# Optimization experiments

Measured on AMD Instinct MI355X. Metric: run time of the kernel, lower is better.

## Reference

```python
import jax, jax.numpy as jnp
import numpy as np

EPS = 1e-5
HEADS = 4


def _ln(x, s, b):
    m = jnp.mean(x, axis=-1, keepdims=True)
    v = jnp.mean(jnp.square(x - m), axis=-1, keepdims=True)
    return (x - m) * jax.lax.rsqrt(v + EPS) * s + b


def _gru(x, Wg, bg, Wcx, bcx, Wch, bch):
    # In this GRUCell the gates depend only on the inputs, so the gate and
    # candidate_x matmuls are precomputed over all timesteps; only the
    # (reset*h) @ Wch matmul is sequential.
    gx = jax.nn.sigmoid(x @ Wg + bg)   # [B,S,2H]
    cx = x @ Wcx + bcx                 # [B,S,H]
    H = Wch.shape[0]

    def step(h, gc):
        g, c = gc
        r, u = jnp.split(g, 2, axis=-1)
        cand = jnp.tanh(c + (r * h) @ Wch + bch)
        h_new = u * h + (1.0 - u) * cand
        return h_new, h_new

    h0 = jnp.zeros((x.shape[0], H), x.dtype)
    _, ys = jax.lax.scan(step, h0, (gx.transpose(1, 0, 2), cx.transpose(1, 0, 2)))
    return ys.transpose(1, 0, 2)


def _attn(x, s, b, Wq, bq, Wk, bk, Wv, bv, Wo, bo):
    skip = x
    xn = _ln(x, s, b)
    B, S, _ = xn.shape
    QKV = Wq.shape[1]
    hd = QKV // HEADS
    q = (xn @ Wq + bq).reshape(B, S, HEADS, hd)
    k = (xn @ Wk + bk).reshape(B, S, HEADS, hd)
    v = (xn @ Wv + bv).reshape(B, S, HEADS, hd)
    scores = jnp.einsum('bqhd,bkhd->bhqk', q, k) / jnp.sqrt(jnp.asarray(hd, x.dtype))
    probs = jax.nn.softmax(scores, axis=-1)
    o = jnp.einsum('bhqk,bkhd->bqhd', probs, v).reshape(B, S, QKV)
    return o @ Wo + bo + skip


def _forward(x_cgm, x_other, W_in, b_in, ln0_s, ln0_b,
             g0_Wg, g0_bg, g0_Wcx, g0_bcx, g0_Wch, g0_bch, ln1_s, ln1_b,
             g1_Wg, g1_bg, g1_Wcx, g1_bcx, g1_Wch, g1_bch, ln2_s, ln2_b,
             aln_s, aln_b, Wq, bq, Wk, bk, Wv, bv, Wo, bo,
             Wd1, bd1, lnd1_s, lnd1_b, Wd2, bd2, lnd2_s, lnd2_b, Wout, bout):
    # input projection + LN
    x = _ln(x_cgm @ W_in + b_in, ln0_s, ln0_b)
    # GRU block 0 (residual: dims match, 256==256)
    y = _gru(x, g0_Wg, g0_bg, g0_Wcx, g0_bcx, g0_Wch, g0_bch)
    x = _ln(y, ln1_s, ln1_b) + x
    # GRU block 1
    y = _gru(x, g1_Wg, g1_bg, g1_Wcx, g1_bcx, g1_Wch, g1_bch)
    x = _ln(y, ln2_s, ln2_b) + x
    # attention block after every 2nd GRU block
    x = _attn(x, aln_s, aln_b, Wq, bq, Wk, bk, Wv, bv, Wo, bo)
    # pool over time, concat static features, dense head (no residuals: dims differ)
    pooled = jnp.mean(x, axis=1)
    c = jnp.concatenate([pooled, x_other], axis=-1)
    c = _ln(jax.nn.relu(c @ Wd1 + bd1), lnd1_s, lnd1_b)
    c = _ln(jax.nn.relu(c @ Wd2 + bd2), lnd2_s, lnd2_b)
    return (c @ Wout + bout).squeeze(-1)


def setup_inputs() -> dict:
    key = jax.random.key(0)
    ks = iter(jax.random.split(key, 64))

    def nrm(shape, scale=1.0):
        return jax.random.normal(next(ks), shape, jnp.float32) * scale

    B, S, Fc, Fo, D, QKV = 64, 288, 16, 32, 256, 64
    inp = {
        'x_cgm': nrm((B, S, Fc)),
        'x_other': nrm((B, Fo)),
        'W_in': nrm((Fc, D), Fc ** -0.5), 'b_in': jnp.zeros((D,), jnp.float32),
        'ln0_s': jnp.ones((D,), jnp.float32), 'ln0_b': jnp.zeros((D,), jnp.float32),
    }
    for p in ('g0', 'g1'):
        inp[p + '_Wg'] = nrm((D, 2 * D), D ** -0.5)
        inp[p + '_bg'] = jnp.zeros((2 * D,), jnp.float32)
        inp[p + '_Wcx'] = nrm((D, D), D ** -0.5)
        inp[p + '_bcx'] = jnp.zeros((D,), jnp.float32)
        inp[p + '_Wch'] = nrm((D, D), D ** -0.5)
        inp[p + '_bch'] = jnp.zeros((D,), jnp.float32)
    for n in ('ln1', 'ln2', 'aln'):
        inp[n + '_s'] = jnp.ones((D,), jnp.float32)
        inp[n + '_b'] = jnp.zeros((D,), jnp.float32)
    for n in ('Wq', 'Wk', 'Wv'):
        inp[n] = nrm((D, QKV), D ** -0.5)
    for n in ('bq', 'bk', 'bv'):
        inp[n] = jnp.zeros((QKV,), jnp.float32)
    inp['Wo'] = nrm((QKV, D), QKV ** -0.5)
    inp['bo'] = jnp.zeros((D,), jnp.float32)
    inp['Wd1'] = nrm((D + Fo, 128), (D + Fo) ** -0.5)
    inp['bd1'] = jnp.zeros((128,), jnp.float32)
    inp['lnd1_s'] = jnp.ones((128,), jnp.float32)
    inp['lnd1_b'] = jnp.zeros((128,), jnp.float32)
    inp['Wd2'] = nrm((128, 64), 128 ** -0.5)
    inp['bd2'] = jnp.zeros((64,), jnp.float32)
    inp['lnd2_s'] = jnp.ones((64,), jnp.float32)
    inp['lnd2_b'] = jnp.zeros((64,), jnp.float32)
    inp['Wout'] = nrm((64, 1), 64 ** -0.5)
    inp['bout'] = jnp.zeros((1,), jnp.float32)
    return inp


def reference(x_cgm, x_other, W_in, b_in, ln0_s, ln0_b,
              g0_Wg, g0_bg, g0_Wcx, g0_bcx, g0_Wch, g0_bch, ln1_s, ln1_b,
              g1_Wg, g1_bg, g1_Wcx, g1_bcx, g1_Wch, g1_bch, ln2_s, ln2_b,
              aln_s, aln_b, Wq, bq, Wk, bk, Wv, bv, Wo, bo,
              Wd1, bd1, lnd1_s, lnd1_b, Wd2, bd2, lnd2_s, lnd2_b, Wout, bout):
    return _forward(x_cgm, x_other, W_in, b_in, ln0_s, ln0_b,
                    g0_Wg, g0_bg, g0_Wcx, g0_bcx, g0_Wch, g0_bch, ln1_s, ln1_b,
                    g1_Wg, g1_bg, g1_Wcx, g1_bcx, g1_Wch, g1_bch, ln2_s, ln2_b,
                    aln_s, aln_b, Wq, bq, Wk, bk, Wv, bv, Wo, bo,
                    Wd1, bd1, lnd1_s, lnd1_b, Wd2, bd2, lnd2_s, lnd2_b, Wout, bout)
```

## Files before the change

### kernel.cpp

```cpp
#include <hip/hip_runtime.h>
#include <hip/hip_bf16.h>
#include <math.h>


#define EPS 1e-5f
constexpr int B_ = 64, S_ = 288, FC = 16, FO = 32, D_ = 256, QKVN = 64, HD = 16;
constexpr int TOK = B_ * S_;
constexpr int NX = TOK * D_;
constexpr int NG = TOK * 512;

typedef short bf16x8 __attribute__((ext_vector_type(8)));
typedef float f32x4 __attribute__((ext_vector_type(4)));

__device__ __forceinline__ short f2bf(float f) {
  __hip_bfloat16 h = __float2bfloat16(f);
  return __builtin_bit_cast(short, h);
}
__device__ __forceinline__ float b2f(__hip_bfloat16 h) {
  return __bfloat162float(h);
}

__device__ __forceinline__ float blk_sum(float v, float* sc) {
  #pragma unroll
  for (int o = 32; o > 0; o >>= 1) v += __shfl_down(v, o, 64);
  int tid = threadIdx.x;
  int wid = tid >> 6, nw = blockDim.x >> 6;
  __syncthreads();
  if ((tid & 63) == 0) sc[wid] = v;
  __syncthreads();
  float s = 0.f;
  for (int w = 0; w < nw; ++w) s += sc[w];
  return s;
}

__global__ __launch_bounds__(256) void prep_w(
    const float* __restrict__ Wg0, const float* __restrict__ Wc0,
    const float* __restrict__ Wg1, const float* __restrict__ Wc1,
    const float* __restrict__ Wq, const float* __restrict__ Wk,
    const float* __restrict__ Wv, const float* __restrict__ Wo,
    __hip_bfloat16* __restrict__ Wt) {
  int seg = blockIdx.y;
  const float* W; int N, K; size_t off;
  switch (seg) {
    case 0: W = Wg0; N = 512; K = 256; off = 0;      break;
    case 1: W = Wc0; N = 256; K = 256; off = 131072; break;
    case 2: W = Wg1; N = 512; K = 256; off = 196608; break;
    case 3: W = Wc1; N = 256; K = 256; off = 327680; break;
    case 4: W = Wq;  N = 64;  K = 256; off = 393216; break;
    case 5: W = Wk;  N = 64;  K = 256; off = 409600; break;
    case 6: W = Wv;  N = 64;  K = 256; off = 425984; break;
    default: W = Wo; N = 256; K = 64;  off = 442368; break;
  }
  int total = N * K;
  for (int i = blockIdx.x * 256 + threadIdx.x; i < total; i += 128 * 256) {
    int n = i / K, k = i - n * K;
    Wt[off + (size_t)n * K + k] = __float2bfloat16(W[(size_t)k * N + n]);
  }
}

__global__ __launch_bounds__(256) void inproj_ln(
    const float* __restrict__ xc, const float* __restrict__ Wi,
    const float* __restrict__ bi, const float* __restrict__ sc_,
    const float* __restrict__ bb, float* __restrict__ X) {
  __shared__ float sc[8];
  int tok = blockIdx.x, j = threadIdx.x;
  const float* xr = xc + tok * FC;
  float acc = bi[j];
  #pragma unroll
  for (int i = 0; i < FC; ++i) acc += xr[i] * Wi[i * D_ + j];
  float m = blk_sum(acc, sc) * (1.f / D_);
  float d = acc - m;
  float var = blk_sum(d * d, sc) * (1.f / D_);
  X[tok * D_ + j] = d * rsqrtf(var + EPS) * sc_[j] + bb[j];
}

__global__ __launch_bounds__(256) void ln_token_res(
    const float* __restrict__ in, const float* __restrict__ sc_,
    const float* __restrict__ bb, const float* __restrict__ resid,
    float* __restrict__ out) {
  __shared__ float sc[8];
  int tok = blockIdx.x, j = threadIdx.x;
  float v = in[tok * D_ + j];
  float m = blk_sum(v, sc) * (1.f / D_);
  float d = v - m;
  float var = blk_sum(d * d, sc) * (1.f / D_);
  out[tok * D_ + j] = d * rsqrtf(var + EPS) * sc_[j] + bb[j] + resid[tok * D_ + j];
}

__global__ __launch_bounds__(256) void ln_ln(
    const float* __restrict__ Y, const float* __restrict__ s2,
    const float* __restrict__ b2, float* __restrict__ X,
    const float* __restrict__ sa, const float* __restrict__ ba,
    __hip_bfloat16* __restrict__ O) {
  __shared__ float sc[8];
  int tok = blockIdx.x, j = threadIdx.x;
  float v = Y[tok * D_ + j];
  float m = blk_sum(v, sc) * (1.f / D_);
  float d = v - m;
  float var = blk_sum(d * d, sc) * (1.f / D_);
  float r = d * rsqrtf(var + EPS) * s2[j] + b2[j] + X[tok * D_ + j];
  X[tok * D_ + j] = r;
  float m2 = blk_sum(r, sc) * (1.f / D_);
  float d2 = r - m2;
  float var2 = blk_sum(d2 * d2, sc) * (1.f / D_);
  O[tok * D_ + j] = __float2bfloat16(d2 * rsqrtf(var2 + EPS) * sa[j] + ba[j]);
}

template <int BN, typename AT, int OBF>
__device__ __forceinline__ void gemm_body(
    const AT* __restrict__ A, const __hip_bfloat16* __restrict__ Wt,
    const float* __restrict__ bias, const float* __restrict__ resid,
    void* __restrict__ OUTv, int N, int bn0, int K, int act, int res,
    short* As, short* Bs) {
  constexpr int BT = BN / 32;
  constexpr int NT16 = BN / 16;
  int tid = threadIdx.x;
  int wave = tid >> 6, lane = tid & 63;
  int quad = lane >> 4, m16 = lane & 15;
  int row0 = blockIdx.x * 128;
  const AT* Ag = A + (size_t)row0 * K;
  const __hip_bfloat16* Wg = Wt + (size_t)bn0 * K;

  f32x4 acc[2][NT16];
  #pragma unroll
  for (int mt = 0; mt < 2; ++mt)
    #pragma unroll
    for (int nt = 0; nt < NT16; ++nt) acc[mt][nt] = (f32x4){0.f, 0.f, 0.f, 0.f};

  float aRf[4][8];
  bf16x8 aRb[4];
  bf16x8 bRb[BT];

  auto loadA = [&](int kk) {
    #pragma unroll
    for (int i = 0; i < 4; ++i) {
      int idx = tid + i * 256;
      int r = idx >> 3, oct = idx & 7;
      if constexpr (sizeof(AT) == 4) {
        const float* p = (const float*)Ag + (size_t)r * K + kk + oct * 8;
        float4 x = *(const float4*)p;
        float4 y = *(const float4*)(p + 4);
        aRf[i][0] = x.x; aRf[i][1] = x.y; aRf[i][2] = x.z; aRf[i][3] = x.w;
        aRf[i][4] = y.x; aRf[i][5] = y.y; aRf[i][6] = y.z; aRf[i][7] = y.w;
      } else {
        aRb[i] = *(const bf16x8*)((const __hip_bfloat16*)Ag +
                                  (size_t)r * K + kk + oct * 8);
      }
    }
  };
  auto loadB = [&](int kk) {
    #pragma unroll
    for (int i = 0; i < BT; ++i) {
      int idx = tid + i * 256;
      int n = idx >> 3, oct = idx & 7;
      bRb[i] = *(const bf16x8*)(Wg + (size_t)n * K + kk + oct * 8);
    }
  };
  auto storeA = [&]() {
    #pragma unroll
    for (int i = 0; i < 4; ++i) {
      int idx = tid + i * 256;
      int r = idx >> 3, oct = idx & 7;
      if constexpr (sizeof(AT) == 4) {
        bf16x8 v;
        #pragma unroll
        for (int j = 0; j < 8; ++j) v[j] = f2bf(aRf[i][j]);
        *(bf16x8*)&As[r * 72 + oct * 8] = v;
      } else {
        *(bf16x8*)&As[r * 72 + oct * 8] = aRb[i];
      }
    }
  };
  auto storeB = [&]() {
    #pragma unroll
    for (int i = 0; i < BT; ++i) {
      int idx = tid + i * 256;
      int n = idx >> 3, oct = idx & 7;
      *(bf16x8*)&Bs[n * 72 + oct * 8] = bRb[i];
    }
  };

  loadA(0); loadB(0);
  for (int kk = 0; kk < K; kk += 64) {
    storeA(); storeB();
    __builtin_amdgcn_s_waitcnt(0xC07F);
    __builtin_amdgcn_s_barrier();
    if (kk + 64 < K) { loadA(kk + 64); loadB(kk + 64); }
    #pragma unroll
    for (int kc = 0; kc < 2; ++kc) {
      bf16x8 af0 = *(const bf16x8*)&As[(wave * 32 + m16) * 72 + kc * 32 + quad * 8];
      bf16x8 af1 = *(const bf16x8*)&As[(wave * 32 + 16 + m16) * 72 + kc * 32 + quad * 8];
      #pragma unroll
      for (int nt = 0; nt < NT16; ++nt) {
        bf16x8 bfr = *(const bf16x8*)&Bs[(nt * 16 + m16) * 72 + kc * 32 + quad * 8];
        acc[0][nt] = __builtin_amdgcn_mfma_f32_16x16x32_bf16(af0, bfr, acc[0][nt], 0, 0, 0);
        acc[1][nt] = __builtin_amdgcn_mfma_f32_16x16x32_bf16(af1, bfr, acc[1][nt], 0, 0, 0);
      }
    }
    __builtin_amdgcn_s_waitcnt(0xC07F);
    __builtin_amdgcn_s_barrier();
  }
  #pragma unroll
  for (int mt = 0; mt < 2; ++mt) {
    #pragma unroll
    for (int nt = 0; nt < NT16; ++nt) {
      int col = bn0 + nt * 16 + m16;
      float bv = bias[col];
      #pragma unroll
      for (int r = 0; r < 4; ++r) {
        int row = row0 + wave * 32 + mt * 16 + quad * 4 + r;
        float v = acc[mt][nt][r] + bv;
        if (act) v = 1.f / (1.f + __expf(-v));
        if (res) v += resid[(size_t)row * N + col];
        if constexpr (OBF) {
          ((__hip_bfloat16*)OUTv)[(size_t)row * N + col] = __float2bfloat16(v);
        } else {
          ((float*)OUTv)[(size_t)row * N + col] = v;
        }
      }
    }
  }
}

__global__ __launch_bounds__(256) void gemm_gru(
    const float* __restrict__ A, const __hip_bfloat16* __restrict__ WtG,
    const float* __restrict__ bg, const __hip_bfloat16* __restrict__ WtC,
    const float* __restrict__ bc, float* __restrict__ G,
    __hip_bfloat16* __restrict__ Cc) {
  __shared__ short As[128 * 72];
  __shared__ short Bs[128 * 72];
  if (blockIdx.y < 4) {
    gemm_body<128, float, 0>(A, WtG, bg, nullptr, (void*)G, 512,
                             blockIdx.y * 128, 256, 1, 0, As, Bs);
  } else {
    gemm_body<128, float, 1>(A, WtC, bc, nullptr, (void*)Cc, 256,
                             (blockIdx.y - 4) * 128, 256, 0, 0, As, Bs);
  }
}

__global__ __launch_bounds__(256) void gemm_qkv(
    const __hip_bfloat16* __restrict__ A, const __hip_bfloat16* __restrict__ Wtq,
    const float* __restrict__ bq, const __hip_bfloat16* __restrict__ Wtk,
    const float* __restrict__ bk, const __hip_bfloat16* __restrict__ Wtv,
    const float* __restrict__ bv, float* __restrict__ Q,
    float* __restrict__ Kb, float* __restrict__ V) {
  __shared__ short As[128 * 72];
  __shared__ short Bs[64 * 72];
  int y = blockIdx.y;
  const __hip_bfloat16* W = (y == 0) ? Wtq : (y == 1) ? Wtk : Wtv;
  const float* bi = (y == 0) ? bq : (y == 1) ? bk : bv;
  float* O = (y == 0) ? Q : (y == 1) ? Kb : V;
  gemm_body<64, __hip_bfloat16, 0>(A, W, bi, nullptr, O, 64, 0, 256, 0, 0, As, Bs);
}

__global__ __launch_bounds__(256) void gemm_proj(
    const __hip_bfloat16* __restrict__ A, const __hip_bfloat16* __restrict__ Wto,
    const float* __restrict__ bi, const float* __restrict__ resid,
    float* __restrict__ O) {
  __shared__ short As[128 * 72];
  __shared__ short Bs[128 * 72];
  gemm_body<128, __hip_bfloat16, 0>(A, Wto, bi, resid, O, 256, blockIdx.y * 128,
                                    64, 0, 1, As, Bs);
}

__global__ __launch_bounds__(512, 2) void gru_scan(
    const float* __restrict__ G, const __hip_bfloat16* __restrict__ C,
    const float* __restrict__ Wch, const float* __restrict__ bch,
    float* __restrict__ Y) {
  __shared__ short vstage[2][256];
  int tid = threadIdx.x;
  int b = blockIdx.x;
  int wave = tid >> 6, lane = tid & 63;
  int quad = lane >> 4, m16 = lane & 15;
  int col0 = 32 * wave + m16;
  int col1 = col0 + 16;

  bf16x8 wfrag[2][8];
  #pragma unroll
  for (int tt = 0; tt < 2; ++tt) {
    int n = (tt == 0) ? col0 : col1;
    #pragma unroll
    for (int c = 0; c < 8; ++c) {
      const float* wp = Wch + (size_t)(32 * c + quad * 8) * D_ + n;
      bf16x8 w;
      #pragma unroll
      for (int j = 0; j < 8; ++j) w[j] = f2bf(wp[(size_t)j * D_]);
      wfrag[tt][c] = w;
    }
  }

  const float* Gp = G + (size_t)b * S_ * 512;
  const __hip_bfloat16* Cp = C + (size_t)b * S_ * 256;
  float* Yp = Y + (size_t)b * S_ * 256;

  float bch0 = bch[col0], bch1 = bch[col1];
  float h0 = 0.f, h1 = 0.f;

  float cu0[4], cu1[4], cc0[4], cc1[4], cr0[4], cr1[4];
  #pragma unroll
  for (int i = 0; i < 4; ++i) {
    cu0[i] = Gp[(size_t)i * 512 + 256 + col0];
    cu1[i] = Gp[(size_t)i * 512 + 256 + col1];
    cc0[i] = b2f(Cp[(size_t)i * 256 + col0]);
    cc1[i] = b2f(Cp[(size_t)i * 256 + col1]);
    cr0[i] = Gp[(size_t)(i + 1) * 512 + col0];
    cr1[i] = Gp[(size_t)(i + 1) * 512 + col1];
  }

  if (tid < 256) vstage[0][tid] = 0;
  __syncthreads();

  constexpr int NGRP = S_ / 4;
  for (int g = 0; g < NGRP; ++g) {
    int gn = (g + 1 < NGRP) ? g + 1 : NGRP - 1;
    const float* Gn = Gp + (size_t)gn * 4 * 512;
    const __hip_bfloat16* Cn = Cp + (size_t)gn * 4 * 256;
    float nu0[4], nu1[4], nc0[4], nc1[4], nr0[4], nr1[4];
    #pragma unroll
    for (int i = 0; i < 4; ++i) {
      nu0[i] = Gn[(size_t)i * 512 + 256 + col0];
      nu1[i] = Gn[(size_t)i * 512 + 256 + col1];
      nc0[i] = b2f(Cn[(size_t)i * 256 + col0]);
      nc1[i] = b2f(Cn[(size_t)i * 256 + col1]);
      int ri = (gn * 4 + i + 1 < S_) ? i + 1 : i;
      nr0[i] = Gn[(size_t)ri * 512 + col0];
      nr1[i] = Gn[(size_t)ri * 512 + col1];
    }
    #pragma unroll
    for (int i = 0; i < 4; ++i) {
      int t = g * 4 + i;
      int buf = t & 1;
      f32x4 A0[4], A1[4];
      #pragma unroll
      for (int j = 0; j < 4; ++j) {
        A0[j] = (f32x4){0.f, 0.f, 0.f, 0.f};
        A1[j] = (f32x4){0.f, 0.f, 0.f, 0.f};
      }
      #pragma unroll
      for (int p = 0; p < 2; ++p) {
        #pragma unroll
        for (int j = 0; j < 4; ++j) {
          int c = p * 4 + j;
          bf16x8 af = *(const bf16x8*)&vstage[buf][(c * 4 + quad) * 8];
          A0[j] = __builtin_amdgcn_mfma_f32_16x16x32_bf16(af, wfrag[0][c], A0[j], 0, 0, 0);
          A1[j] = __builtin_amdgcn_mfma_f32_16x16x32_bf16(af, wfrag[1][c], A1[j], 0, 0, 0);
        }
      }
      float s0 = cc0[i] + bch0 + ((A0[0][0] + A0[1][0]) + (A0[2][0] + A0[3][0]));
      float s1 = cc1[i] + bch1 + ((A1[0][0] + A1[1][0]) + (A1[2][0] + A1[3][0]));
      float e0 = __expf(2.f * s0), e1 = __expf(2.f * s1);
      float cand0 = 1.f - 2.f / (e0 + 1.f);
      float cand1 = 1.f - 2.f / (e1 + 1.f);
      h0 = cu0[i] * h0 + (1.f - cu0[i]) * cand0;
      h1 = cu1[i] * h1 + (1.f - cu1[i]) * cand1;
      short v0 = f2bf(cr0[i] * h0), v1 = f2bf(cr1[i] * h1);
      if (quad == 0) {
        Yp[(size_t)t * 256 + col0] = h0;
        Yp[(size_t)t * 256 + col1] = h1;
        vstage[buf ^ 1][col0] = v0;
        vstage[buf ^ 1][col1] = v1;
      }
      __builtin_amdgcn_s_waitcnt(0xC07F);
      __builtin_amdgcn_s_barrier();
    }
    #pragma unroll
    for (int i = 0; i < 4; ++i) {
      cu0[i] = nu0[i]; cu1[i] = nu1[i];
      cc0[i] = nc0[i]; cc1[i] = nc1[i];
      cr0[i] = nr0[i]; cr1[i] = nr1[i];
    }
  }
}

__global__ __launch_bounds__(320) void attn(
    const float* __restrict__ Q, const float* __restrict__ Kv,
    const float* __restrict__ V, __hip_bfloat16* __restrict__ AO) {
  __shared__ float Kl[S_ * HD];
  __shared__ float Vl[S_ * HD];
  int b = blockIdx.x, hh = blockIdx.y;
  int tid = threadIdx.x;
  int hoff = hh * HD;
  for (int idx = tid; idx < S_ * HD; idx += 320) {
    int row = idx >> 4, d = idx & 15;
    Kl[idx] = Kv[((size_t)(b * S_ + row)) * QKVN + hoff + d];
    Vl[idx] = V[((size_t)(b * S_ + row)) * QKVN + hoff + d];
  }
  __syncthreads();
  if (tid >= S_) return;
  const float* qp = Q + ((size_t)(b * S_ + tid)) * QKVN + hoff;
  float4 q0 = *(const float4*)(qp + 0);
  float4 q1 = *(const float4*)(qp + 4);
  float4 q2 = *(const float4*)(qp + 8);
  float4 q3 = *(const float4*)(qp + 12);
  float m = -1e30f, l = 0.f;
  float4 o0 = {0, 0, 0, 0}, o1 = {0, 0, 0, 0}, o2 = {0, 0, 0, 0},
         o3 = {0, 0, 0, 0};
  for (int k = 0; k < S_; ++k) {
    const float4* kp = (const float4*)&Kl[k * HD];
    float4 k0 = kp[0], k1 = kp[1], k2 = kp[2], k3 = kp[3];
    float s = q0.x * k0.x + q0.y * k0.y + q0.z * k0.z + q0.w * k0.w +
              q1.x * k1.x + q1.y * k1.y + q1.z * k1.z + q1.w * k1.w +
              q2.x * k2.x + q2.y * k2.y + q2.z * k2.z + q2.w * k2.w +
              q3.x * k3.x + q3.y * k3.y + q3.z * k3.z + q3.w * k3.w;
    s *= 0.25f;
    float mn = fmaxf(m, s);
    float corr = __expf(m - mn);
    float p = __expf(s - mn);
    l = l * corr + p;
    const float4* vp = (const float4*)&Vl[k * HD];
    float4 v0 = vp[0], v1 = vp[1], v2 = vp[2], v3 = vp[3];
    o0.x = o0.x * corr + p * v0.x; o0.y = o0.y * corr + p * v0.y;
    o0.z = o0.z * corr + p * v0.z; o0.w = o0.w * corr + p * v0.w;
    o1.x = o1.x * corr + p * v1.x; o1.y = o1.y * corr + p * v1.y;
    o1.z = o1.z * corr + p * v1.z; o1.w = o1.w * corr + p * v1.w;
    o2.x = o2.x * corr + p * v2.x; o2.y = o2.y * corr + p * v2.y;
    o2.z = o2.z * corr + p * v2.z; o2.w = o2.w * corr + p * v2.w;
    o3.x = o3.x * corr + p * v3.x; o3.y = o3.y * corr + p * v3.y;
    o3.z = o3.z * corr + p * v3.z; o3.w = o3.w * corr + p * v3.w;
    m = mn;
  }
  float inv = 1.f / l;
  __hip_bfloat16* op = AO + ((size_t)(b * S_ + tid)) * QKVN + hoff;
  bf16x8 w0, w1;
  w0[0] = f2bf(o0.x * inv); w0[1] = f2bf(o0.y * inv);
  w0[2] = f2bf(o0.z * inv); w0[3] = f2bf(o0.w * inv);
  w0[4] = f2bf(o1.x * inv); w0[5] = f2bf(o1.y * inv);
  w0[6] = f2bf(o1.z * inv); w0[7] = f2bf(o1.w * inv);
  w1[0] = f2bf(o2.x * inv); w1[1] = f2bf(o2.y * inv);
  w1[2] = f2bf(o2.z * inv); w1[3] = f2bf(o2.w * inv);
  w1[4] = f2bf(o3.x * inv); w1[5] = f2bf(o3.y * inv);
  w1[6] = f2bf(o3.z * inv); w1[7] = f2bf(o3.w * inv);
  *(bf16x8*)op = w0;
  *(bf16x8*)(op + 8) = w1;
}

__global__ __launch_bounds__(256) void head(
    const float* __restrict__ X, const float* __restrict__ xo,
    const float* __restrict__ Wd1, const float* __restrict__ bd1,
    const float* __restrict__ s1, const float* __restrict__ b1,
    const float* __restrict__ Wd2, const float* __restrict__ bd2,
    const float* __restrict__ s2, const float* __restrict__ b2,
    const float* __restrict__ Wout, const float* __restrict__ bout,
    float* __restrict__ out) {
  __shared__ float c[D_ + FO];
  __shared__ float h1[128];
  __shared__ float sc[8];
  int b = blockIdx.x, tid = threadIdx.x;
  {
    float acc = 0.f;
    const float* xp = X + (size_t)b * S_ * D_ + tid;
    #pragma unroll 4
    for (int t = 0; t < S_; ++t) acc += xp[(size_t)t * D_];
    c[tid] = acc * (1.f / S_);
  }
  if (tid < FO) c[D_ + tid] = xo[b * FO + tid];
  __syncthreads();
  float v = 0.f;
  if (tid < 128) {
    v = bd1[tid];
    for (int k = 0; k < D_ + FO; ++k) v += c[k] * Wd1[k * 128 + tid];
    v = fmaxf(v, 0.f);
  }
  float m = blk_sum(tid < 128 ? v : 0.f, sc) * (1.f / 128.f);
  float d = v - m;
  float var = blk_sum(tid < 128 ? d * d : 0.f, sc) * (1.f / 128.f);
  if (tid < 128) h1[tid] = d * rsqrtf(var + EPS) * s1[tid] + b1[tid];
  __syncthreads();
  float v2 = 0.f;
  if (tid < 64) {
    v2 = bd2[tid];
    for (int k = 0; k < 128; ++k) v2 += h1[k] * Wd2[k * 64 + tid];
    v2 = fmaxf(v2, 0.f);
  }
  float m2 = blk_sum(tid < 64 ? v2 : 0.f, sc) * (1.f / 64.f);
  float d2v = v2 - m2;
  float var2 = blk_sum(tid < 64 ? d2v * d2v : 0.f, sc) * (1.f / 64.f);
  float hv = (tid < 64) ? (d2v * rsqrtf(var2 + EPS) * s2[tid] + b2[tid]) : 0.f;
  float p = (tid < 64) ? hv * Wout[tid] : 0.f;
  float tot = blk_sum(p, sc);
  if (tid == 0) out[b] = tot + bout[0];
}

extern "C" void kernel_launch(void* const* d_in, const int* in_sizes, int n_in,
                              void* d_out, int out_size, void* d_ws,
                              size_t ws_size, hipStream_t stream) {
  const float* x_cgm = (const float*)d_in[0];
  const float* x_other = (const float*)d_in[1];
  const float* W_in = (const float*)d_in[2];
  const float* b_in = (const float*)d_in[3];
  const float* ln0_s = (const float*)d_in[4];
  const float* ln0_b = (const float*)d_in[5];
  const float* g0_Wg = (const float*)d_in[6];
  const float* g0_bg = (const float*)d_in[7];
  const float* g0_Wcx = (const float*)d_in[8];
  const float* g0_bcx = (const float*)d_in[9];
  const float* g0_Wch = (const float*)d_in[10];
  const float* g0_bch = (const float*)d_in[11];
  const float* g1_Wg = (const float*)d_in[12];
  const float* g1_bg = (const float*)d_in[13];
  const float* g1_Wcx = (const float*)d_in[14];
  const float* g1_bcx = (const float*)d_in[15];
  const float* g1_Wch = (const float*)d_in[16];
  const float* g1_bch = (const float*)d_in[17];
  const float* ln1_s = (const float*)d_in[18];
  const float* ln1_b = (const float*)d_in[19];
  const float* ln2_s = (const float*)d_in[20];
  const float* ln2_b = (const float*)d_in[21];
  const float* aln_s = (const float*)d_in[22];
  const float* aln_b = (const float*)d_in[23];
  const float* Wq = (const float*)d_in[24];
  const float* Wk = (const float*)d_in[25];
  const float* Wv = (const float*)d_in[26];
  const float* bq = (const float*)d_in[27];
  const float* bk = (const float*)d_in[28];
  const float* bv = (const float*)d_in[29];
  const float* Wo = (const float*)d_in[30];
  const float* bo = (const float*)d_in[31];
  const float* Wd1 = (const float*)d_in[32];
  const float* bd1 = (const float*)d_in[33];
  const float* lnd1_s = (const float*)d_in[34];
  const float* lnd1_b = (const float*)d_in[35];
  const float* Wd2 = (const float*)d_in[36];
  const float* bd2 = (const float*)d_in[37];
  const float* lnd2_s = (const float*)d_in[38];
  const float* lnd2_b = (const float*)d_in[39];
  const float* Wout = (const float*)d_in[40];
  const float* bout = (const float*)d_in[41];
  (void)in_sizes; (void)n_in; (void)out_size; (void)ws_size;

  float* ws = (float*)d_ws;
  float* X = ws;
  float* Yb = ws + NX;
  float* Gb = ws + 2 * NX;
  __hip_bfloat16* Cb = (__hip_bfloat16*)(ws + 2 * NX + NG);
  __hip_bfloat16* Wt = (__hip_bfloat16*)(ws + 2 * NX + NG + NX / 2);
  float* Qb = Gb;
  float* Kbuf = Qb + TOK * QKVN;
  float* Vbuf = Qb + 2 * TOK * QKVN;
  __hip_bfloat16* Obuf = Cb;
  __hip_bfloat16* AO = (__hip_bfloat16*)Yb;

  __hip_bfloat16* Wt_g0 = Wt + 0;
  __hip_bfloat16* Wt_c0 = Wt + 131072;
  __hip_bfloat16* Wt_g1 = Wt + 196608;
  __hip_bfloat16* Wt_c1 = Wt + 327680;
  __hip_bfloat16* Wt_q  = Wt + 393216;
  __hip_bfloat16* Wt_k  = Wt + 409600;
  __hip_bfloat16* Wt_v  = Wt + 425984;
  __hip_bfloat16* Wt_o  = Wt + 442368;

  const int MB = TOK / 128;

  prep_w<<<dim3(128, 8), 256, 0, stream>>>(g0_Wg, g0_Wcx, g1_Wg, g1_Wcx,
                                           Wq, Wk, Wv, Wo, Wt);
  inproj_ln<<<TOK, 256, 0, stream>>>(x_cgm, W_in, b_in, ln0_s, ln0_b, X);

  gemm_gru<<<dim3(MB, 6), 256, 0, stream>>>(X, Wt_g0, g0_bg, Wt_c0, g0_bcx, Gb, Cb);
  gru_scan<<<B_, 512, 0, stream>>>(Gb, Cb, g0_Wch, g0_bch, Yb);
  ln_token_res<<<TOK, 256, 0, stream>>>(Yb, ln1_s, ln1_b, X, X);

  gemm_gru<<<dim3(MB, 6), 256, 0, stream>>>(X, Wt_g1, g1_bg, Wt_c1, g1_bcx, Gb, Cb);
  gru_scan<<<B_, 512, 0, stream>>>(Gb, Cb, g1_Wch, g1_bch, Yb);

  ln_ln<<<TOK, 256, 0, stream>>>(Yb, ln2_s, ln2_b, X, aln_s, aln_b, Obuf);

  gemm_qkv<<<dim3(MB, 3), 256, 0, stream>>>(Obuf, Wt_q, bq, Wt_k, bk, Wt_v, bv,
                                            Qb, Kbuf, Vbuf);
  attn<<<dim3(B_, 4), 320, 0, stream>>>(Qb, Kbuf, Vbuf, AO);
  gemm_proj<<<dim3(MB, 2), 256, 0, stream>>>(AO, Wt_o, bo, X, X);

  head<<<B_, 256, 0, stream>>>(X, x_other, Wd1, bd1, lnd1_s, lnd1_b,
                               Wd2, bd2, lnd2_s, lnd2_b, Wout, bout,
                               (float*)d_out);
}
```

Measured before the change: 698.4 us.

## Halve GRU scan block to 4 waves with 64 columns per wave

The GRU recurrence kernel now runs with 256 threads per batch element instead of 512. Each wave owns 64 hidden columns (four MFMA column tiles), and the K reduction is split into two independent accumulator chains. Per-step prefetch of gate and candidate values replaces the 4-step grouped prefetch. The aim is cheaper per-step barriers with fewer waves and more MFMA work per wave. In exchange each wave carries more register state and a longer serial chain of MFMAs per step.

```diff
diff --git a/kernel.cpp b/kernel.cpp
--- a/kernel.cpp
+++ b/kernel.cpp
@@ -263,7 +263,7 @@
                                     64, 0, 1, As, Bs);
 }
 
-__global__ __launch_bounds__(512, 2) void gru_scan(
+__global__ __launch_bounds__(256, 2) void gru_scan(
     const float* __restrict__ G, const __hip_bfloat16* __restrict__ C,
     const float* __restrict__ Wch, const float* __restrict__ bch,
     float* __restrict__ Y) {
@@ -272,20 +272,20 @@
   int b = blockIdx.x;
   int wave = tid >> 6, lane = tid & 63;
   int quad = lane >> 4, m16 = lane & 15;
-  int col0 = 32 * wave + m16;
-  int col1 = col0 + 16;
-
-  bf16x8 wfrag[2][8];
-  #pragma unroll
-  for (int tt = 0; tt < 2; ++tt) {
-    int n = (tt == 0) ? col0 : col1;
+  int col[4];
+  #pragma unroll
+  for (int j = 0; j < 4; ++j) col[j] = 64 * wave + 16 * j + m16;
+
+  bf16x8 wfrag[4][8];
+  #pragma unroll
+  for (int j = 0; j < 4; ++j) {
     #pragma unroll
     for (int c = 0; c < 8; ++c) {
-      const float* wp = Wch + (size_t)(32 * c + quad * 8) * D_ + n;
+      const float* wp = Wch + (size_t)(32 * c + quad * 8) * D_ + col[j];
       bf16x8 w;
       #pragma unroll
-      for (int j = 0; j < 8; ++j) w[j] = f2bf(wp[(size_t)j * D_]);
-      wfrag[tt][c] = w;
+      for (int jj = 0; jj < 8; ++jj) w[jj] = f2bf(wp[(size_t)jj * D_]);
+      wfrag[j][c] = w;
     }
   }
 
@@ -293,82 +293,66 @@
   const __hip_bfloat16* Cp = C + (size_t)b * S_ * 256;
   float* Yp = Y + (size_t)b * S_ * 256;
 
-  float bch0 = bch[col0], bch1 = bch[col1];
-  float h0 = 0.f, h1 = 0.f;
-
-  float cu0[4], cu1[4], cc0[4], cc1[4], cr0[4], cr1[4];
-  #pragma unroll
-  for (int i = 0; i < 4; ++i) {
-    cu0[i] = Gp[(size_t)i * 512 + 256 + col0];
-    cu1[i] = Gp[(size_t)i * 512 + 256 + col1];
-    cc0[i] = b2f(Cp[(size_t)i * 256 + col0]);
-    cc1[i] = b2f(Cp[(size_t)i * 256 + col1]);
-    cr0[i] = Gp[(size_t)(i + 1) * 512 + col0];
-    cr1[i] = Gp[(size_t)(i + 1) * 512 + col1];
-  }
-
-  if (tid < 256) vstage[0][tid] = 0;
+  float bchv[4], h[4], cu[4], cc[4], cr[4];
+  #pragma unroll
+  for (int j = 0; j < 4; ++j) {
+    bchv[j] = bch[col[j]];
+    h[j] = 0.f;
+    cu[j] = Gp[256 + col[j]];
+    cc[j] = b2f(Cp[col[j]]);
+    cr[j] = Gp[512 + col[j]];
+  }
+
+  vstage[0][tid] = 0;
   __syncthreads();
 
-  constexpr int NGRP = S_ / 4;
-  for (int g = 0; g < NGRP; ++g) {
-    int gn = (g + 1 < NGRP) ? g + 1 : NGRP - 1;
-    const float* Gn = Gp + (size_t)gn * 4 * 512;
-    const __hip_bfloat16* Cn = Cp + (size_t)gn * 4 * 256;
-    float nu0[4], nu1[4], nc0[4], nc1[4], nr0[4], nr1[4];
-    #pragma unroll
-    for (int i = 0; i < 4; ++i) {
-      nu0[i] = Gn[(size_t)i * 512 + 256 + col0];
-      nu1[i] = Gn[(size_t)i * 512 + 256 + col1];
-      nc0[i] = b2f(Cn[(size_t)i * 256 + col0]);
-      nc1[i] = b2f(Cn[(size_t)i * 256 + col1]);
-      int ri = (gn * 4 + i + 1 < S_) ? i + 1 : i;
-      nr0[i] = Gn[(size_t)ri * 512 + col0];
-      nr1[i] = Gn[(size_t)ri * 512 + col1];
-    }
-    #pragma unroll
-    for (int i = 0; i < 4; ++i) {
-      int t = g * 4 + i;
-      int buf = t & 1;
-      f32x4 A0[4], A1[4];
+  for (int t = 0; t < S_; ++t) {
+    int buf = t & 1;
+    f32x4 accA[4], accB[4];
+    #pragma unroll
+    for (int j = 0; j < 4; ++j) {
+      accA[j] = (f32x4){0.f, 0.f, 0.f, 0.f};
+      accB[j] = (f32x4){0.f, 0.f, 0.f, 0.f};
+    }
+    #pragma unroll
+    for (int c = 0; c < 4; ++c) {
+      bf16x8 afA = *(const bf16x8*)&vstage[buf][(c * 4 + quad) * 8];
+      bf16x8 afB = *(const bf16x8*)&vstage[buf][((c + 4) * 4 + quad) * 8];
       #pragma unroll
       for (int j = 0; j < 4; ++j) {
-        A0[j] = (f32x4){0.f, 0.f, 0.f, 0.f};
-        A1[j] = (f32x4){0.f, 0.f, 0.f, 0.f};
+        accA[j] = __builtin_amdgcn_mfma_f32_16x16x32_bf16(afA, wfrag[j][c], accA[j], 0, 0, 0);
+        accB[j] = __builtin_amdgcn_mfma_f32_16x16x32_bf16(afB, wfrag[j][c + 4], accB[j], 0, 0, 0);
       }
+    }
+    int tl = (t + 1 < S_) ? t + 1 : S_ - 1;
+    int tr = (t + 2 < S_) ? t + 2 : S_ - 1;
+    float nu[4], nc[4], nr[4];
+    #pragma unroll
+    for (int j = 0; j < 4; ++j) {
+      nu[j] = Gp[(size_t)tl * 512 + 256 + col[j]];
+      nc[j] = b2f(Cp[(size_t)tl * 256 + col[j]]);
+      nr[j] = Gp[(size_t)tr * 512 + col[j]];
+    }
+    short v[4];
+    #pragma unroll
+    for (int j = 0; j < 4; ++j) {
+      float s = cc[j] + bchv[j] + accA[j][0] + accB[j][0];
+      float e = __expf(2.f * s);
+      float cand = 1.f - 2.f / (e + 1.f);
+      h[j] = cu[j] * h[j] + (1.f - cu[j]) * cand;
+      v[j] = f2bf(cr[j] * h[j]);
+    }
+    if (quad == 0) {
       #pragma unroll
-      for (int p = 0; p < 2; ++p) {
-        #pragma unroll
-        for (int j = 0; j < 4; ++j) {
-          int c = p * 4 + j;
-          bf16x8 af = *(const bf16x8*)&vstage[buf][(c * 4 + quad) * 8];
-          A0[j] = __builtin_amdgcn_mfma_f32_16x16x32_bf16(af, wfrag[0][c], A0[j], 0, 0, 0);
-          A1[j] = __builtin_amdgcn_mfma_f32_16x16x32_bf16(af, wfrag[1][c], A1[j], 0, 0, 0);
-        }
+      for (int j = 0; j < 4; ++j) {
+        Yp[(size_t)t * 256 + col[j]] = h[j];
+        vstage[buf ^ 1][col[j]] = v[j];
       }
-      float s0 = cc0[i] + bch0 + ((A0[0][0] + A0[1][0]) + (A0[2][0] + A0[3][0]));
-      float s1 = cc1[i] + bch1 + ((A1[0][0] + A1[1][0]) + (A1[2][0] + A1[3][0]));
-      float e0 = __expf(2.f * s0), e1 = __expf(2.f * s1);
-      float cand0 = 1.f - 2.f / (e0 + 1.f);
-      float cand1 = 1.f - 2.f / (e1 + 1.f);
-      h0 = cu0[i] * h0 + (1.f - cu0[i]) * cand0;
-      h1 = cu1[i] * h1 + (1.f - cu1[i]) * cand1;
-      short v0 = f2bf(cr0[i] * h0), v1 = f2bf(cr1[i] * h1);
-      if (quad == 0) {
-        Yp[(size_t)t * 256 + col0] = h0;
-        Yp[(size_t)t * 256 + col1] = h1;
-        vstage[buf ^ 1][col0] = v0;
-        vstage[buf ^ 1][col1] = v1;
-      }
-      __builtin_amdgcn_s_waitcnt(0xC07F);
-      __builtin_amdgcn_s_barrier();
-    }
-    #pragma unroll
-    for (int i = 0; i < 4; ++i) {
-      cu0[i] = nu0[i]; cu1[i] = nu1[i];
-      cc0[i] = nc0[i]; cc1[i] = nc1[i];
-      cr0[i] = nr0[i]; cr1[i] = nr1[i];
-    }
+    }
+    #pragma unroll
+    for (int j = 0; j < 4; ++j) { cu[j] = nu[j]; cc[j] = nc[j]; cr[j] = nr[j]; }
+    __builtin_amdgcn_s_waitcnt(0xC07F);
+    __builtin_amdgcn_s_barrier();
   }
 }
 
@@ -556,11 +540,11 @@
   inproj_ln<<<TOK, 256, 0, stream>>>(x_cgm, W_in, b_in, ln0_s, ln0_b, X);
 
   gemm_gru<<<dim3(MB, 6), 256, 0, stream>>>(X, Wt_g0, g0_bg, Wt_c0, g0_bcx, Gb, Cb);
-  gru_scan<<<B_, 512, 0, stream>>>(Gb, Cb, g0_Wch, g0_bch, Yb);
+  gru_scan<<<B_, 256, 0, stream>>>(Gb, Cb, g0_Wch, g0_bch, Yb);
   ln_token_res<<<TOK, 256, 0, stream>>>(Yb, ln1_s, ln1_b, X, X);
 
   gemm_gru<<<dim3(MB, 6), 256, 0, stream>>>(X, Wt_g1, g1_bg, Wt_c1, g1_bcx, Gb, Cb);
-  gru_scan<<<B_, 512, 0, stream>>>(Gb, Cb, g1_Wch, g1_bch, Yb);
+  gru_scan<<<B_, 256, 0, stream>>>(Gb, Cb, g1_Wch, g1_bch, Yb);
 
   ln_ln<<<TOK, 256, 0, stream>>>(Yb, ln2_s, ln2_b, X, aln_s, aln_b, Obuf);
 
```

Result: slower. 787.3 us (+12.7%).
